# Optimization experiments

Measured on AMD Instinct MI355X. Metric: run time of the kernel, lower is better.

## Reference

```python
import jax, jax.numpy as jnp
import numpy as np

HIDDEN = 4096
N_HEADS = 32
N_KV_HEADS = 8
HEAD_DIM = HIDDEN // N_HEADS  # 128
Q_SIZE = N_HEADS * HEAD_DIM
KV_SIZE = N_KV_HEADS * HEAD_DIM
ROPE_THETA = 10000.0
EPS = 1e-5
SCALE = HEAD_DIM ** -0.5


def _headwise_layernorm(x, weight, eps):
    # x: [B,S,H,D], weight: [H,D]; LayerNorm over last dim (head_dim), fp32 math
    xf = x.astype(jnp.float32)
    mean = xf.mean(-1, keepdims=True)
    var = jnp.square(xf - mean).mean(-1, keepdims=True)
    y = (xf - mean) * jax.lax.rsqrt(var + eps)
    return (weight.astype(jnp.float32) * y).astype(x.dtype)


def _rope_gptj(x, positions):
    # non-neox (GPT-J) style: rotate interleaved pairs. x: [B,S,H,D]
    half = HEAD_DIM // 2
    inv_freq = 1.0 / (ROPE_THETA ** (jnp.arange(0, HEAD_DIM, 2, dtype=jnp.float32) / HEAD_DIM))
    ang = positions.astype(jnp.float32)[..., None] * inv_freq  # [B,S,half]
    cos = jnp.cos(ang)[:, :, None, :]  # [B,S,1,half]
    sin = jnp.sin(ang)[:, :, None, :]
    x1 = x[..., 0::2]
    x2 = x[..., 1::2]
    o1 = x1 * cos - x2 * sin
    o2 = x2 * cos + x1 * sin
    # re-interleave
    out = jnp.stack([o1, o2], axis=-1).reshape(x.shape)
    return out.astype(x.dtype)


def setup_inputs() -> dict:
    key = jax.random.key(0)
    k1, k2, k3, k4 = jax.random.split(key, 4)
    B, S = 2, 2048
    positions = jnp.tile(jnp.arange(S, dtype=jnp.int32)[None, :], (B, 1))
    hidden_states = jax.random.normal(k1, (B, S, HIDDEN), dtype=jnp.float32)
    Wqkv = jax.random.normal(k2, (HIDDEN, Q_SIZE + 2 * KV_SIZE), dtype=jnp.float32) * (HIDDEN ** -0.5)
    Wo = jax.random.normal(k3, (Q_SIZE, HIDDEN), dtype=jnp.float32) * (Q_SIZE ** -0.5)
    kq, kk = jax.random.split(k4)
    q_norm_w = jnp.ones((N_HEADS, HEAD_DIM), jnp.float32) + 0.02 * jax.random.normal(kq, (N_HEADS, HEAD_DIM))
    k_norm_w = jnp.ones((N_KV_HEADS, HEAD_DIM), jnp.float32) + 0.02 * jax.random.normal(kk, (N_KV_HEADS, HEAD_DIM))
    return {"positions": positions, "hidden_states": hidden_states, "Wqkv": Wqkv,
            "q_norm_w": q_norm_w, "k_norm_w": k_norm_w, "Wo": Wo}


def reference(positions, hidden_states, Wqkv, q_norm_w, k_norm_w, Wo):
    B, S, _ = hidden_states.shape
    qkv = hidden_states @ Wqkv  # [B,S,Q+2KV]
    q, k, v = jnp.split(qkv, [Q_SIZE, Q_SIZE + KV_SIZE], axis=-1)
    q = q.reshape(B, S, N_HEADS, HEAD_DIM)
    k = k.reshape(B, S, N_KV_HEADS, HEAD_DIM)
    v = v.reshape(B, S, N_KV_HEADS, HEAD_DIM)
    # per-head qk-norm
    q = _headwise_layernorm(q, q_norm_w, EPS)
    k = _headwise_layernorm(k, k_norm_w, EPS)
    # non-neox RoPE
    q = _rope_gptj(q, positions)
    k = _rope_gptj(k, positions)
    # GQA: repeat kv heads
    n_rep = N_HEADS // N_KV_HEADS
    k = jnp.repeat(k, n_rep, axis=2)  # [B,S,H,D]
    v = jnp.repeat(v, n_rep, axis=2)
    scores = jnp.einsum('bqhd,bkhd->bhqk', q, k) * SCALE
    causal = jnp.tril(jnp.ones((S, S), dtype=bool))
    scores = jnp.where(causal[None, None], scores, jnp.finfo(scores.dtype).min)
    probs = jax.nn.softmax(scores, axis=-1)
    attn = jnp.einsum('bhqk,bkhd->bqhd', probs, v).reshape(B, S, Q_SIZE)
    return attn @ Wo
```

## Files before the change

kernel.cpp:

```cpp
#include <hip/hip_runtime.h>
#include <hip/hip_bf16.h>
#include <cstdint>

typedef unsigned short u16;
typedef unsigned int u32;
typedef __attribute__((ext_vector_type(8))) short bf16x8;
typedef __attribute__((ext_vector_type(4))) float f32x4;
typedef __attribute__((ext_vector_type(16))) float f32x16;
typedef __attribute__((ext_vector_type(4))) unsigned int u32x4;

#define HIDDEN 4096
#define NH 32
#define NKV 8
#define HD 128
#define QSZ 4096
#define KVSZ 1024
#define QKV_N 6144
#define SEQ 2048
#define NB 2
#define NTOK (NB*SEQ)
#define ATT_SCALE 0.08838834764831845f
#define LOG2E 1.4426950408889634f
#define LN_EPS 1e-5f
#define THRD 12.0f

__device__ __forceinline__ u16 f2bf(float f) {
  union { float f; u32 u; } a; a.f = f;
  u32 r = a.u + 0x7fffu + ((a.u >> 16) & 1u);
  return (u16)(r >> 16);
}
__device__ __forceinline__ float bf2f(u16 h) {
  union { u32 u; float f; } a; a.u = ((u32)h) << 16;
  return a.f;
}

__device__ __forceinline__ void gload_lds16(const void* g, void* l) {
  __builtin_amdgcn_global_load_lds(
      (const __attribute__((address_space(1))) void*)g,
      (__attribute__((address_space(3))) void*)l,
      16, 0, 0);
}

__global__ __launch_bounds__(256)
void conv_f32_bf16(const float* __restrict__ in, u16* __restrict__ out, int n8) {
  int i = blockIdx.x * 256 + threadIdx.x;
  if (i >= n8) return;
  const float4* p = (const float4*)in + (size_t)i * 2;
  float4 v0 = p[0], v1 = p[1];
  u32x4 o;
  o.x = (u32)f2bf(v0.x) | ((u32)f2bf(v0.y) << 16);
  o.y = (u32)f2bf(v0.z) | ((u32)f2bf(v0.w) << 16);
  o.z = (u32)f2bf(v1.x) | ((u32)f2bf(v1.y) << 16);
  o.w = (u32)f2bf(v1.z) | ((u32)f2bf(v1.w) << 16);
  ((u32x4*)out)[i] = o;
}

__global__ __launch_bounds__(256)
void transp_f32_bf16(const float* __restrict__ in, u16* __restrict__ out, int R, int C) {
  __shared__ float tile[32][33];
  int c0 = blockIdx.x << 5, r0 = blockIdx.y << 5;
  int tx = threadIdx.x & 31, ty = threadIdx.x >> 5;
  #pragma unroll
  for (int j = 0; j < 32; j += 8)
    tile[ty + j][tx] = in[(long)(r0 + ty + j) * C + c0 + tx];
  __syncthreads();
  #pragma unroll
  for (int j = 0; j < 32; j += 8)
    out[(long)(c0 + ty + j) * R + r0 + tx] = f2bf(tile[tx][ty + j]);
}

template<typename OutT>
__global__ __launch_bounds__(512, 2)
void gemm_bt6(const u16* __restrict__ A, const u16* __restrict__ Bt,
              OutT* __restrict__ C, int N, int K) {
  extern __shared__ char smem[];
  const int t = threadIdx.x;
  const int lane = t & 63, w = t >> 6;
  const int wr = w >> 2, wc = w & 3;
  const int l31 = lane & 31, l7 = lane & 7, g2 = lane >> 5;
  const int bm = blockIdx.y, bn = blockIdx.x;

  const int ciA0 = t, ciA1 = t + 512;
  const u16* AgS0 = A + (long)(bm * 128 + (ciA0 >> 3)) * K + (((ciA0 & 7) ^ ((ciA0 >> 3) & 7)) << 3);
  const u16* AgS1 = A + (long)(bm * 128 + (ciA1 >> 3)) * K + (((ciA1 & 7) ^ ((ciA1 >> 3) & 7)) << 3);
  const u16* BgS0;
  const u16* BgS1;
  const u16* BgS2;
  const u16* BgS3;
  {
    int ci0 = t, ci1 = t + 512, ci2 = t + 1024, ci3 = t + 1536;
    BgS0 = Bt + (long)(bn * 256 + (ci0 >> 3)) * K + (((ci0 & 7) ^ ((ci0 >> 3) & 7)) << 3);
    BgS1 = Bt + (long)(bn * 256 + (ci1 >> 3)) * K + (((ci1 & 7) ^ ((ci1 >> 3) & 7)) << 3);
    BgS2 = Bt + (long)(bn * 256 + (ci2 >> 3)) * K + (((ci2 & 7) ^ ((ci2 >> 3) & 7)) << 3);
    BgS3 = Bt + (long)(bn * 256 + (ci3 >> 3)) * K + (((ci3 & 7) ^ ((ci3 >> 3) & 7)) << 3);
  }
  const int dA0 = (w * 64) * 16;
  const int dA1 = (512 + w * 64) * 16;
  const int dB0 = 16384 + (w * 64) * 16;
  const int dB1 = 16384 + (512 + w * 64) * 16;
  const int dB2 = 16384 + (1024 + w * 64) * 16;
  const int dB3 = 16384 + (1536 + w * 64) * 16;

  const int arow0 = (wr * 64 + l31) * 128;
  const int brow0 = 16384 + (wc * 64 + l31) * 128;

  f32x16 acc[2][2];
  #pragma unroll
  for (int i = 0; i < 2; ++i)
    #pragma unroll
    for (int j = 0; j < 2; ++j)
      #pragma unroll
      for (int r = 0; r < 16; ++r) acc[i][j][r] = 0.f;

  const int nt = K >> 6;
  char* cbase = smem;
  char* nbase = smem + 49152;
  char* sbase = smem + 98304;

  #define STAGE6(dst, koff) { \
    gload_lds16(AgS0 + (koff), dst + dA0);  gload_lds16(AgS1 + (koff), dst + dA1); \
    gload_lds16(BgS0 + (koff), dst + dB0);  gload_lds16(BgS1 + (koff), dst + dB1); \
    gload_lds16(BgS2 + (koff), dst + dB2);  gload_lds16(BgS3 + (koff), dst + dB3); }

  STAGE6(cbase, 0);
  STAGE6(nbase, 64);
  asm volatile("s_waitcnt vmcnt(6)" ::: "memory");
  __builtin_amdgcn_s_barrier();
  __builtin_amdgcn_sched_barrier(0);

  #define READ_KK(dst, kkv) { \
    const int pcb = (((kkv) * 2 + g2) ^ l7) * 16; \
    dst[0] = *(const bf16x8*)(cbase + arow0 + pcb); \
    dst[1] = *(const bf16x8*)(cbase + arow0 + 32 * 128 + pcb); \
    dst[2] = *(const bf16x8*)(cbase + brow0 + pcb); \
    dst[3] = *(const bf16x8*)(cbase + brow0 + 32 * 128 + pcb); }
  #define MFMA_KK(f) { \
    __builtin_amdgcn_s_setprio(1); \
    acc[0][0] = __builtin_amdgcn_mfma_f32_32x32x16_bf16(f[0], f[2], acc[0][0], 0, 0, 0); \
    acc[0][1] = __builtin_amdgcn_mfma_f32_32x32x16_bf16(f[0], f[3], acc[0][1], 0, 0, 0); \
    acc[1][0] = __builtin_amdgcn_mfma_f32_32x32x16_bf16(f[1], f[2], acc[1][0], 0, 0, 0); \
    acc[1][1] = __builtin_amdgcn_mfma_f32_32x32x16_bf16(f[1], f[3], acc[1][1], 0, 0, 0); \
    __builtin_amdgcn_s_setprio(0); }

  for (int tt = 0; tt < nt; ++tt) {
    const long sk = (long)((tt + 2 < nt) ? (tt + 2) : (nt - 1)) * 64;
    STAGE6(sbase, sk);
    bf16x8 fA[4], fB[4], fC[4], fD[4];
    READ_KK(fA, 0);
    READ_KK(fB, 1);
    MFMA_KK(fA);
    READ_KK(fC, 2);
    MFMA_KK(fB);
    READ_KK(fD, 3);
    MFMA_KK(fC);
    MFMA_KK(fD);
    asm volatile("s_waitcnt vmcnt(6)" ::: "memory");
    __builtin_amdgcn_s_barrier();
    __builtin_amdgcn_sched_barrier(0);
    char* tmp = cbase; cbase = nbase; nbase = sbase; sbase = tmp;
  }
  #undef READ_KK
  #undef MFMA_KK
  #undef STAGE6

  #pragma unroll
  for (int mf = 0; mf < 2; ++mf)
    #pragma unroll
    for (int nf = 0; nf < 2; ++nf)
      #pragma unroll
      for (int r = 0; r < 16; ++r) {
        long row = bm * 128 + wr * 64 + mf * 32 + (r & 3) + 8 * (r >> 2) + 4 * g2;
        long col = bn * 256 + wc * 64 + nf * 32 + l31;
        float v = acc[mf][nf][r];
        if constexpr (sizeof(OutT) == 2) C[row * N + col] = f2bf(v);
        else                             C[row * N + col] = v;
      }
}

__device__ __forceinline__ void ln_rope_head(const u16* __restrict__ src,
                                             const float* __restrict__ wgt,
                                             u16* __restrict__ dst,
                                             int lane, float sa, float ca, float scale) {
  u32 xr = *(const u32*)(src + 2 * lane);
  float x1 = bf2f((u16)(xr & 0xffffu)), x2 = bf2f((u16)(xr >> 16));
  float ssum = x1 + x2;
  #pragma unroll
  for (int off = 1; off < 64; off <<= 1) ssum += __shfl_xor(ssum, off);
  float mean = ssum * (1.0f / 128.0f);
  float e1 = x1 - mean, e2 = x2 - mean;
  float vv = e1 * e1 + e2 * e2;
  #pragma unroll
  for (int off = 1; off < 64; off <<= 1) vv += __shfl_xor(vv, off);
  float rstd = rsqrtf(vv * (1.0f / 128.0f) + LN_EPS);
  float y1 = e1 * rstd * wgt[2 * lane];
  float y2 = e2 * rstd * wgt[2 * lane + 1];
  float o1 = (y1 * ca - y2 * sa) * scale;
  float o2 = (y2 * ca + y1 * sa) * scale;
  *(u32*)(dst + 2 * lane) = (u32)f2bf(o1) | ((u32)f2bf(o2) << 16);
}

__global__ __launch_bounds__(512)
void ln_rope(const u16* __restrict__ qkv, const int* __restrict__ pos,
             const float* __restrict__ qw, const float* __restrict__ kw,
             u16* __restrict__ qo, u16* __restrict__ ko) {
  const int s = blockIdx.x, b = blockIdx.y;
  const int t = threadIdx.x, lane = t & 63, w = t >> 6;
  const long base = (long)(b * SEQ + s) * QKV_N;
  const int p = pos[b * SEQ + s];
  const float expo = (float)(2 * lane) * (1.0f / 128.0f);
  const float inv_freq = exp2f(-expo * 13.287712379549449f);
  float sa, ca;
  sincosf((float)p * inv_freq, &sa, &ca);
  #pragma unroll
  for (int hh = 0; hh < 4; ++hh) {
    int h = w + hh * 8;
    ln_rope_head(qkv + base + h * HD, qw + h * HD,
                 qo + (((long)b * NH + h) * SEQ + s) * HD, lane, sa, ca,
                 ATT_SCALE * LOG2E);
  }
  ln_rope_head(qkv + base + QSZ + w * HD, kw + w * HD,
               ko + (((long)b * NKV + w) * SEQ + s) * HD, lane, sa, ca, 1.0f);
}

__global__ __launch_bounds__(256)
void v_transp(const u16* __restrict__ qkv, u16* __restrict__ vt) {
  __shared__ u16 tile[32][33];
  int s0 = blockIdx.x * 32, d0 = blockIdx.y * 32;
  int bk = blockIdx.z;
  int b = bk >> 3, kvh = bk & 7;
  int tx = threadIdx.x & 31, ty = threadIdx.x >> 5;
  const u16* src = qkv + ((long)(b * SEQ) + s0) * QKV_N + QSZ + KVSZ + kvh * HD + d0;
  #pragma unroll
  for (int j = 0; j < 32; j += 8)
    tile[ty + j][tx] = src[(long)(ty + j) * QKV_N + tx];
  __syncthreads();
  u16* dst = vt + (((long)bk) * HD + d0) * SEQ + s0;
  #pragma unroll
  for (int j = 0; j < 32; j += 8)
    dst[(long)(ty + j) * SEQ + tx] = tile[tx][ty + j];
}

__global__ __launch_bounds__(512, 2)
void flash_attn2(const u16* __restrict__ Qg, const u16* __restrict__ Kg,
                 const u16* __restrict__ Vtg, u16* __restrict__ Og) {
  const int lin = blockIdx.x;
  const int b = lin >> 8;
  const int rem = lin & 255;
  const int h = rem >> 3;
  const int q3 = rem & 7;
  const int qt = b ? (7 - q3) : q3;
  const int kvh = h >> 2;
  const int t = threadIdx.x, lane = t & 63, w = t >> 6;
  const int hh = lane >> 5, l31 = lane & 31;
  const int wq0 = qt * 256 + w * 32;
  const int q = wq0 + l31;

  __shared__ u16 Klds[2][64 * 128];
  __shared__ u16 Vlds[2][128 * 64];

  const u16* Qbase = Qg + (((long)b * NH + h) * SEQ + q) * HD + hh * 8;
  bf16x8 qf[8];
  #pragma unroll
  for (int ks = 0; ks < 8; ++ks) qf[ks] = *(const bf16x8*)(Qbase + ks * 16);

  f32x16 o[4];
  #pragma unroll
  for (int i = 0; i < 4; ++i)
    #pragma unroll
    for (int r = 0; r < 16; ++r) o[i][r] = 0.f;
  float m = -1e30f, l = 0.f;

  const u16* Kbase = Kg + ((long)b * NKV + kvh) * (long)SEQ * HD;
  const u16* Vtbase = Vtg + ((long)b * NKV + kvh) * (long)HD * SEQ;
  const int nt = qt * 4 + 4;

  auto STAGE = [&](int buf, int kt) {
    const int kv0 = kt * 64;
    #pragma unroll
    for (int i = 0; i < 2; ++i) {
      int c = t + i * 512;
      int kv = c >> 4, cc = c & 15;
      int cl = (cc & 8) | ((cc ^ kv) & 7);
      gload_lds16(Kbase + (long)(kv0 + kv) * HD + cl * 8,
                  (char*)(&Klds[buf][0]) + (i * 512 + w * 64) * 16);
    }
    #pragma unroll
    for (int i = 0; i < 2; ++i) {
      int c = t + i * 512;
      int d = c >> 3, cc = c & 7;
      int cl = cc ^ (d & 7);
      gload_lds16(Vtbase + (long)d * SEQ + kv0 + cl * 8,
                  (char*)(&Vlds[buf][0]) + (i * 512 + w * 64) * 16);
    }
  };

  STAGE(0, 0);
  __syncthreads();
  int cur = 0;
  for (int kt = 0; kt < nt; ++kt) {
    const int kv0 = kt * 64;
    if (kt + 1 < nt) STAGE(cur ^ 1, kt + 1);
    if (kv0 <= wq0 + 31) {
      const char* Kb = (const char*)(&Klds[cur][0]);
      const char* Vb = (const char*)(&Vlds[cur][0]);
      f32x16 st[2];
      #pragma unroll
      for (int tt = 0; tt < 2; ++tt)
        #pragma unroll
        for (int r = 0; r < 16; ++r) st[tt][r] = 0.f;
      __builtin_amdgcn_s_setprio(1);
      #pragma unroll
      for (int tt = 0; tt < 2; ++tt) {
        if (kv0 + tt * 32 <= wq0 + 31) {
          #pragma unroll
          for (int ks = 0; ks < 8; ++ks) {
            int ch = ks * 2 + hh;
            int pc = (ch & 8) | ((ch ^ l31) & 7);
            bf16x8 kf = *(const bf16x8*)(Kb + (tt * 32 + l31) * 256 + pc * 16);
            st[tt] = __builtin_amdgcn_mfma_f32_32x32x16_bf16(kf, qf[ks], st[tt], 0, 0, 0);
          }
        }
      }
      __builtin_amdgcn_s_setprio(0);
      if (kv0 + 63 > wq0) {
        #pragma unroll
        for (int tt = 0; tt < 2; ++tt)
          #pragma unroll
          for (int r = 0; r < 16; ++r) {
            int kva = kv0 + tt * 32 + (r & 3) + 8 * (r >> 2) + 4 * hh;
            if (kva > q) st[tt][r] = -1e30f;
          }
      }
      float p0 = -1e30f, p1 = -1e30f, p2 = -1e30f, p3 = -1e30f;
      #pragma unroll
      for (int tt = 0; tt < 2; ++tt)
        #pragma unroll
        for (int r = 0; r < 16; r += 4) {
          p0 = fmaxf(p0, st[tt][r]);
          p1 = fmaxf(p1, st[tt][r + 1]);
          p2 = fmaxf(p2, st[tt][r + 2]);
          p3 = fmaxf(p3, st[tt][r + 3]);
        }
      float mx = fmaxf(fmaxf(p0, p1), fmaxf(p2, p3));
      mx = fmaxf(mx, __shfl_xor(mx, 32));
      if (!__all(mx - m <= THRD)) {
        float mn = fmaxf(m, mx);
        float sc = exp2f(m - mn);
        m = mn;
        float scr[16];
        #pragma unroll
        for (int r = 0; r < 16; ++r)
          scr[r] = __shfl(sc, (r & 3) + 8 * (r >> 2) + 4 * hh);
        #pragma unroll
        for (int db = 0; db < 4; ++db)
          #pragma unroll
          for (int r = 0; r < 16; ++r) o[db][r] *= scr[r];
        l *= sc;
      }
      float s0 = 0.f, s1 = 0.f, s2 = 0.f, s3 = 0.f;
      #pragma unroll
      for (int tt = 0; tt < 2; ++tt)
        #pragma unroll
        for (int r = 0; r < 16; r += 4) {
          float e0 = exp2f(st[tt][r] - m);
          float e1 = exp2f(st[tt][r + 1] - m);
          float e2 = exp2f(st[tt][r + 2] - m);
          float e3 = exp2f(st[tt][r + 3] - m);
          st[tt][r] = e0; st[tt][r + 1] = e1; st[tt][r + 2] = e2; st[tt][r + 3] = e3;
          s0 += e0; s1 += e1; s2 += e2; s3 += e3;
        }
      float rs = (s0 + s1) + (s2 + s3);
      rs += __shfl_xor(rs, 32);
      l += rs;
      bf16x8 pa[4];
      #pragma unroll
      for (int k4 = 0; k4 < 4; ++k4) {
        int s8 = (k4 & 1) * 8, tt = k4 >> 1;
        u32 x0 = (u32)f2bf(st[tt][s8 + 0]) | ((u32)f2bf(st[tt][s8 + 1]) << 16);
        u32 x1 = (u32)f2bf(st[tt][s8 + 2]) | ((u32)f2bf(st[tt][s8 + 3]) << 16);
        u32 y0 = (u32)f2bf(st[tt][s8 + 4]) | ((u32)f2bf(st[tt][s8 + 5]) << 16);
        u32 y1 = (u32)f2bf(st[tt][s8 + 6]) | ((u32)f2bf(st[tt][s8 + 7]) << 16);
        u32 x0s = (u32)__shfl_xor((int)x0, 32), x1s = (u32)__shfl_xor((int)x1, 32);
        u32 y0s = (u32)__shfl_xor((int)y0, 32), y1s = (u32)__shfl_xor((int)y1, 32);
        union { u32 u[4]; bf16x8 v; } pk;
        pk.u[0] = hh ? y0s : x0;
        pk.u[1] = hh ? y1s : x1;
        pk.u[2] = hh ? y0 : x0s;
        pk.u[3] = hh ? y1 : x1s;
        pa[k4] = pk.v;
      }
      __builtin_amdgcn_s_setprio(1);
      #pragma unroll
      for (int k4 = 0; k4 < 4; ++k4)
        #pragma unroll
        for (int db = 0; db < 4; ++db) {
          int ch = k4 * 2 + hh;
          int pcc = ch ^ (l31 & 7);
          bf16x8 vf = *(const bf16x8*)(Vb + (db * 32 + l31) * 128 + pcc * 16);
          o[db] = __builtin_amdgcn_mfma_f32_32x32x16_bf16(pa[k4], vf, o[db], 0, 0, 0);
        }
      __builtin_amdgcn_s_setprio(0);
    }
    __syncthreads();
    cur ^= 1;
  }
  float linv = 1.0f / l;
  float li[16];
  #pragma unroll
  for (int r = 0; r < 16; ++r)
    li[r] = __shfl(linv, (r & 3) + 8 * (r >> 2) + 4 * hh);
  #pragma unroll
  for (int db = 0; db < 4; ++db)
    #pragma unroll
    for (int r = 0; r < 16; ++r) {
      int qr = wq0 + (r & 3) + 8 * (r >> 2) + 4 * hh;
      Og[((long)b * SEQ + qr) * QSZ + h * HD + db * 32 + l31] = f2bf(o[db][r] * li[r]);
    }
}

extern "C" void kernel_launch(void* const* d_in, const int* in_sizes, int n_in,
                              void* d_out, int out_size, void* d_ws, size_t ws_size,
                              hipStream_t stream) {
  const int*   positions = (const int*)d_in[0];
  const float* hidden    = (const float*)d_in[1];
  const float* Wqkv      = (const float*)d_in[2];
  const float* qnw       = (const float*)d_in[3];
  const float* knw       = (const float*)d_in[4];
  const float* Wo        = (const float*)d_in[5];
  float* out = (float*)d_out;
  char* ws = (char*)d_ws;
  const size_t MB = 1024 * 1024;
  u16* hbf   = (u16*)(ws + 0);
  u16* WqkvT = (u16*)(ws + 32 * MB);
  u16* qkvb  = (u16*)(ws + 80 * MB);
  u16* q_arr = (u16*)(ws + 0);
  u16* k_arr = (u16*)(ws + 32 * MB);
  u16* vt_arr= (u16*)(ws + 40 * MB);
  u16* WoT   = (u16*)(ws + 48 * MB);
  u16* Oarr  = (u16*)(ws + 80 * MB);

  const int GEMM_LDS = 3 * 49152;
  (void)hipFuncSetAttribute((const void*)&gemm_bt6<u16>,
        hipFuncAttributeMaxDynamicSharedMemorySize, GEMM_LDS);
  (void)hipFuncSetAttribute((const void*)&gemm_bt6<float>,
        hipFuncAttributeMaxDynamicSharedMemorySize, GEMM_LDS);

  conv_f32_bf16<<<dim3(NTOK * HIDDEN / 8 / 256), 256, 0, stream>>>(hidden, hbf, NTOK * HIDDEN / 8);
  transp_f32_bf16<<<dim3(QKV_N / 32, HIDDEN / 32), 256, 0, stream>>>(Wqkv, WqkvT, HIDDEN, QKV_N);
  gemm_bt6<u16><<<dim3(QKV_N / 256, NTOK / 128), 512, GEMM_LDS, stream>>>(hbf, WqkvT, qkvb, QKV_N, HIDDEN);
  ln_rope<<<dim3(SEQ, NB), 512, 0, stream>>>(qkvb, positions, qnw, knw, q_arr, k_arr);
  v_transp<<<dim3(SEQ / 32, HD / 32, NB * NKV), 256, 0, stream>>>(qkvb, vt_arr);
  transp_f32_bf16<<<dim3(HIDDEN / 32, QSZ / 32), 256, 0, stream>>>(Wo, WoT, QSZ, HIDDEN);
  flash_attn2<<<dim3(512), 512, 0, stream>>>(q_arr, k_arr, vt_arr, Oarr);
  gemm_bt6<float><<<dim3(HIDDEN / 256, NTOK / 128), 512, GEMM_LDS, stream>>>(Oarr, WoT, out, HIDDEN, QSZ);
}
```

Baseline: 584.7 us.

## Split GEMM main loop into two ping-pong phases with interleaved loads and barriers

Restructures the GEMM inner loop into two half-steps. Each half issues half of the global-to-LDS prefetch loads together with LDS fragment reads, then runs a barrier-delimited MFMA cluster at raised priority, in the style of a ping-pong schedule across the waves of two co-resident blocks. The aim is to spread memory issue across the iteration and overlap it with matrix math. The cost is two extra workgroup barriers per iteration and more sensitivity to scheduling.

```diff
diff --git a/kernel.cpp b/kernel.cpp
--- a/kernel.cpp
+++ b/kernel.cpp
@@ -71,7 +71,7 @@
 
 template<typename OutT>
 __global__ __launch_bounds__(512, 2)
-void gemm_bt6(const u16* __restrict__ A, const u16* __restrict__ Bt,
+void gemm_bt7(const u16* __restrict__ A, const u16* __restrict__ Bt,
               OutT* __restrict__ C, int N, int K) {
   extern __shared__ char smem[];
   const int t = threadIdx.x;
@@ -135,28 +135,43 @@
     dst[2] = *(const bf16x8*)(cbase + brow0 + pcb); \
     dst[3] = *(const bf16x8*)(cbase + brow0 + 32 * 128 + pcb); }
   #define MFMA_KK(f) { \
-    __builtin_amdgcn_s_setprio(1); \
     acc[0][0] = __builtin_amdgcn_mfma_f32_32x32x16_bf16(f[0], f[2], acc[0][0], 0, 0, 0); \
     acc[0][1] = __builtin_amdgcn_mfma_f32_32x32x16_bf16(f[0], f[3], acc[0][1], 0, 0, 0); \
     acc[1][0] = __builtin_amdgcn_mfma_f32_32x32x16_bf16(f[1], f[2], acc[1][0], 0, 0, 0); \
-    acc[1][1] = __builtin_amdgcn_mfma_f32_32x32x16_bf16(f[1], f[3], acc[1][1], 0, 0, 0); \
-    __builtin_amdgcn_s_setprio(0); }
+    acc[1][1] = __builtin_amdgcn_mfma_f32_32x32x16_bf16(f[1], f[3], acc[1][1], 0, 0, 0); }
 
   for (int tt = 0; tt < nt; ++tt) {
     const long sk = (long)((tt + 2 < nt) ? (tt + 2) : (nt - 1)) * 64;
-    STAGE6(sbase, sk);
-    bf16x8 fA[4], fB[4], fC[4], fD[4];
+    bf16x8 fA[4], fB[4];
     READ_KK(fA, 0);
     READ_KK(fB, 1);
+    gload_lds16(AgS0 + sk, sbase + dA0);
+    gload_lds16(AgS1 + sk, sbase + dA1);
+    gload_lds16(BgS0 + sk, sbase + dB0);
+    __builtin_amdgcn_sched_barrier(0);
+    __builtin_amdgcn_s_barrier();
+    __builtin_amdgcn_sched_barrier(0);
+    __builtin_amdgcn_s_setprio(1);
     MFMA_KK(fA);
-    READ_KK(fC, 2);
     MFMA_KK(fB);
-    READ_KK(fD, 3);
-    MFMA_KK(fC);
-    MFMA_KK(fD);
+    __builtin_amdgcn_s_setprio(0);
+    __builtin_amdgcn_sched_barrier(0);
+    __builtin_amdgcn_s_barrier();
+    READ_KK(fA, 2);
+    READ_KK(fB, 3);
+    gload_lds16(BgS1 + sk, sbase + dB1);
+    gload_lds16(BgS2 + sk, sbase + dB2);
+    gload_lds16(BgS3 + sk, sbase + dB3);
     asm volatile("s_waitcnt vmcnt(6)" ::: "memory");
+    __builtin_amdgcn_sched_barrier(0);
     __builtin_amdgcn_s_barrier();
     __builtin_amdgcn_sched_barrier(0);
+    __builtin_amdgcn_s_setprio(1);
+    MFMA_KK(fA);
+    MFMA_KK(fB);
+    __builtin_amdgcn_s_setprio(0);
+    __builtin_amdgcn_sched_barrier(0);
+    __builtin_amdgcn_s_barrier();
     char* tmp = cbase; cbase = nbase; nbase = sbase; sbase = tmp;
   }
   #undef READ_KK
@@ -440,17 +455,17 @@
   u16* Oarr  = (u16*)(ws + 80 * MB);
 
   const int GEMM_LDS = 3 * 49152;
-  (void)hipFuncSetAttribute((const void*)&gemm_bt6<u16>,
+  (void)hipFuncSetAttribute((const void*)&gemm_bt7<u16>,
         hipFuncAttributeMaxDynamicSharedMemorySize, GEMM_LDS);
-  (void)hipFuncSetAttribute((const void*)&gemm_bt6<float>,
+  (void)hipFuncSetAttribute((const void*)&gemm_bt7<float>,
         hipFuncAttributeMaxDynamicSharedMemorySize, GEMM_LDS);
 
   conv_f32_bf16<<<dim3(NTOK * HIDDEN / 8 / 256), 256, 0, stream>>>(hidden, hbf, NTOK * HIDDEN / 8);
   transp_f32_bf16<<<dim3(QKV_N / 32, HIDDEN / 32), 256, 0, stream>>>(Wqkv, WqkvT, HIDDEN, QKV_N);
-  gemm_bt6<u16><<<dim3(QKV_N / 256, NTOK / 128), 512, GEMM_LDS, stream>>>(hbf, WqkvT, qkvb, QKV_N, HIDDEN);
+  gemm_bt7<u16><<<dim3(QKV_N / 256, NTOK / 128), 512, GEMM_LDS, stream>>>(hbf, WqkvT, qkvb, QKV_N, HIDDEN);
   ln_rope<<<dim3(SEQ, NB), 512, 0, stream>>>(qkvb, positions, qnw, knw, q_arr, k_arr);
   v_transp<<<dim3(SEQ / 32, HD / 32, NB * NKV), 256, 0, stream>>>(qkvb, vt_arr);
   transp_f32_bf16<<<dim3(HIDDEN / 32, QSZ / 32), 256, 0, stream>>>(Wo, WoT, QSZ, HIDDEN);
   flash_attn2<<<dim3(512), 512, 0, stream>>>(q_arr, k_arr, vt_arr, Oarr);
-  gemm_bt6<float><<<dim3(HIDDEN / 256, NTOK / 128), 512, GEMM_LDS, stream>>>(Oarr, WoT, out, HIDDEN, QSZ);
-}
+  gemm_bt7<float><<<dim3(HIDDEN / 256, NTOK / 128), 512, GEMM_LDS, stream>>>(Oarr, WoT, out, HIDDEN, QSZ);
+}
```

Result: no change. 594.1 us (+1.6%).

## Add 256x256 double-buffered output GEMM and pair causal q-tiles in attention

Applied to the files above, without the earlier changes.

Adds a new gemm_bt4 kernel for the output projection. It uses 256x256 tiles with double buffering, and each wave computes a 128x64 block, which raises data reuse per LDS load. The attention kernel now processes two causal q-tiles per block: a long one (7-qp) and a short one (qp). This balances the work and halves the grid to 256 blocks. The risks are more register pressure in the bigger GEMM, lower occupancy (the grid becomes 16x16=256 blocks), and less latency hiding in attention from the smaller grid.

```diff
diff --git a/kernel.cpp b/kernel.cpp
--- a/kernel.cpp
+++ b/kernel.cpp
@@ -128,13 +128,13 @@
   __builtin_amdgcn_s_barrier();
   __builtin_amdgcn_sched_barrier(0);
 
-  #define READ_KK(dst, kkv) { \
+  #define READ_KK6(dst, kkv) { \
     const int pcb = (((kkv) * 2 + g2) ^ l7) * 16; \
     dst[0] = *(const bf16x8*)(cbase + arow0 + pcb); \
     dst[1] = *(const bf16x8*)(cbase + arow0 + 32 * 128 + pcb); \
     dst[2] = *(const bf16x8*)(cbase + brow0 + pcb); \
     dst[3] = *(const bf16x8*)(cbase + brow0 + 32 * 128 + pcb); }
-  #define MFMA_KK(f) { \
+  #define MFMA_KK6(f) { \
     __builtin_amdgcn_s_setprio(1); \
     acc[0][0] = __builtin_amdgcn_mfma_f32_32x32x16_bf16(f[0], f[2], acc[0][0], 0, 0, 0); \
     acc[0][1] = __builtin_amdgcn_mfma_f32_32x32x16_bf16(f[0], f[3], acc[0][1], 0, 0, 0); \
@@ -146,21 +146,21 @@
     const long sk = (long)((tt + 2 < nt) ? (tt + 2) : (nt - 1)) * 64;
     STAGE6(sbase, sk);
     bf16x8 fA[4], fB[4], fC[4], fD[4];
-    READ_KK(fA, 0);
-    READ_KK(fB, 1);
-    MFMA_KK(fA);
-    READ_KK(fC, 2);
-    MFMA_KK(fB);
-    READ_KK(fD, 3);
-    MFMA_KK(fC);
-    MFMA_KK(fD);
+    READ_KK6(fA, 0);
+    READ_KK6(fB, 1);
+    MFMA_KK6(fA);
+    READ_KK6(fC, 2);
+    MFMA_KK6(fB);
+    READ_KK6(fD, 3);
+    MFMA_KK6(fC);
+    MFMA_KK6(fD);
     asm volatile("s_waitcnt vmcnt(6)" ::: "memory");
     __builtin_amdgcn_s_barrier();
     __builtin_amdgcn_sched_barrier(0);
     char* tmp = cbase; cbase = nbase; nbase = sbase; sbase = tmp;
   }
-  #undef READ_KK
-  #undef MFMA_KK
+  #undef READ_KK6
+  #undef MFMA_KK6
   #undef STAGE6
 
   #pragma unroll
@@ -170,6 +170,113 @@
       #pragma unroll
       for (int r = 0; r < 16; ++r) {
         long row = bm * 128 + wr * 64 + mf * 32 + (r & 3) + 8 * (r >> 2) + 4 * g2;
+        long col = bn * 256 + wc * 64 + nf * 32 + l31;
+        float v = acc[mf][nf][r];
+        if constexpr (sizeof(OutT) == 2) C[row * N + col] = f2bf(v);
+        else                             C[row * N + col] = v;
+      }
+}
+
+template<typename OutT>
+__global__ __launch_bounds__(512, 2)
+void gemm_bt4(const u16* __restrict__ A, const u16* __restrict__ Bt,
+              OutT* __restrict__ C, int N, int K) {
+  extern __shared__ char smem[];
+  const int t = threadIdx.x;
+  const int lane = t & 63, w = t >> 6;
+  const int wr = w >> 2, wc = w & 3;
+  const int l31 = lane & 31, g2 = lane >> 5;
+  const int bm = blockIdx.y, bn = blockIdx.x;
+
+  const u16* pA[4]; const u16* pB[4];
+  int dS[4];
+  #pragma unroll
+  for (int i = 0; i < 4; ++i) {
+    int ci = t + i * 512;
+    int row = ci >> 3;
+    int c = (ci & 7) ^ (row & 7);
+    pA[i] = A  + (long)(bm * 256 + row) * K + (c << 3);
+    pB[i] = Bt + (long)(bn * 256 + row) * K + (c << 3);
+    dS[i] = (i * 512 + w * 64) * 16;
+  }
+
+  const int arowB = (wr * 128 + l31) * 128;
+  const int browB = 32768 + (wc * 64 + l31) * 128;
+
+  f32x16 acc[4][2];
+  #pragma unroll
+  for (int i = 0; i < 4; ++i)
+    #pragma unroll
+    for (int j = 0; j < 2; ++j)
+      #pragma unroll
+      for (int r = 0; r < 16; ++r) acc[i][j][r] = 0.f;
+
+  const int nt = K >> 6;
+  char* cb = smem;
+  char* sb = smem + 65536;
+
+  #pragma unroll
+  for (int i = 0; i < 4; ++i) gload_lds16(pA[i], cb + dS[i]);
+  #pragma unroll
+  for (int i = 0; i < 4; ++i) gload_lds16(pB[i], cb + 32768 + dS[i]);
+  asm volatile("s_waitcnt vmcnt(0)" ::: "memory");
+  __builtin_amdgcn_s_barrier();
+  __builtin_amdgcn_sched_barrier(0);
+
+  #define READ_KK4(dst, kkv) { \
+    const int pcb = ((((kkv) * 2 + g2)) ^ (l31 & 7)) << 4; \
+    dst[0] = *(const bf16x8*)(cb + arowB + pcb); \
+    dst[1] = *(const bf16x8*)(cb + arowB + 4096 + pcb); \
+    dst[2] = *(const bf16x8*)(cb + arowB + 8192 + pcb); \
+    dst[3] = *(const bf16x8*)(cb + arowB + 12288 + pcb); \
+    dst[4] = *(const bf16x8*)(cb + browB + pcb); \
+    dst[5] = *(const bf16x8*)(cb + browB + 4096 + pcb); }
+  #define MFMA_KK4(f) { \
+    __builtin_amdgcn_s_setprio(1); \
+    acc[0][0] = __builtin_amdgcn_mfma_f32_32x32x16_bf16(f[0], f[4], acc[0][0], 0, 0, 0); \
+    acc[0][1] = __builtin_amdgcn_mfma_f32_32x32x16_bf16(f[0], f[5], acc[0][1], 0, 0, 0); \
+    acc[1][0] = __builtin_amdgcn_mfma_f32_32x32x16_bf16(f[1], f[4], acc[1][0], 0, 0, 0); \
+    acc[1][1] = __builtin_amdgcn_mfma_f32_32x32x16_bf16(f[1], f[5], acc[1][1], 0, 0, 0); \
+    acc[2][0] = __builtin_amdgcn_mfma_f32_32x32x16_bf16(f[2], f[4], acc[2][0], 0, 0, 0); \
+    acc[2][1] = __builtin_amdgcn_mfma_f32_32x32x16_bf16(f[2], f[5], acc[2][1], 0, 0, 0); \
+    acc[3][0] = __builtin_amdgcn_mfma_f32_32x32x16_bf16(f[3], f[4], acc[3][0], 0, 0, 0); \
+    acc[3][1] = __builtin_amdgcn_mfma_f32_32x32x16_bf16(f[3], f[5], acc[3][1], 0, 0, 0); \
+    __builtin_amdgcn_s_setprio(0); }
+
+  for (int tt = 0; tt < nt; ++tt) {
+    const long sk = (long)((tt + 1 < nt) ? (tt + 1) : (nt - 1)) * 64;
+    bf16x8 f0[6], f1[6];
+    READ_KK4(f0, 0);
+    gload_lds16(pA[0] + sk, sb + dS[0]);
+    gload_lds16(pA[1] + sk, sb + dS[1]);
+    READ_KK4(f1, 1);
+    gload_lds16(pA[2] + sk, sb + dS[2]);
+    gload_lds16(pA[3] + sk, sb + dS[3]);
+    MFMA_KK4(f0);
+    gload_lds16(pB[0] + sk, sb + 32768 + dS[0]);
+    gload_lds16(pB[1] + sk, sb + 32768 + dS[1]);
+    MFMA_KK4(f1);
+    READ_KK4(f0, 2);
+    gload_lds16(pB[2] + sk, sb + 32768 + dS[2]);
+    gload_lds16(pB[3] + sk, sb + 32768 + dS[3]);
+    MFMA_KK4(f0);
+    READ_KK4(f1, 3);
+    MFMA_KK4(f1);
+    asm volatile("s_waitcnt vmcnt(0)" ::: "memory");
+    __builtin_amdgcn_s_barrier();
+    __builtin_amdgcn_sched_barrier(0);
+    char* tmp = cb; cb = sb; sb = tmp;
+  }
+  #undef READ_KK4
+  #undef MFMA_KK4
+
+  #pragma unroll
+  for (int mf = 0; mf < 4; ++mf)
+    #pragma unroll
+    for (int nf = 0; nf < 2; ++nf)
+      #pragma unroll
+      for (int r = 0; r < 16; ++r) {
+        long row = bm * 256 + wr * 128 + mf * 32 + (r & 3) + 8 * (r >> 2) + 4 * g2;
         long col = bn * 256 + wc * 64 + nf * 32 + l31;
         float v = acc[mf][nf][r];
         if constexpr (sizeof(OutT) == 2) C[row * N + col] = f2bf(v);
@@ -241,38 +348,22 @@
 }
 
 __global__ __launch_bounds__(512, 2)
-void flash_attn2(const u16* __restrict__ Qg, const u16* __restrict__ Kg,
+void flash_attn3(const u16* __restrict__ Qg, const u16* __restrict__ Kg,
                  const u16* __restrict__ Vtg, u16* __restrict__ Og) {
   const int lin = blockIdx.x;
-  const int b = lin >> 8;
-  const int rem = lin & 255;
-  const int h = rem >> 3;
-  const int q3 = rem & 7;
-  const int qt = b ? (7 - q3) : q3;
+  const int b = lin >> 7;
+  const int rem = lin & 127;
+  const int h = rem >> 2;
+  const int qp = rem & 3;
   const int kvh = h >> 2;
   const int t = threadIdx.x, lane = t & 63, w = t >> 6;
   const int hh = lane >> 5, l31 = lane & 31;
-  const int wq0 = qt * 256 + w * 32;
-  const int q = wq0 + l31;
 
   __shared__ u16 Klds[2][64 * 128];
   __shared__ u16 Vlds[2][128 * 64];
 
-  const u16* Qbase = Qg + (((long)b * NH + h) * SEQ + q) * HD + hh * 8;
-  bf16x8 qf[8];
-  #pragma unroll
-  for (int ks = 0; ks < 8; ++ks) qf[ks] = *(const bf16x8*)(Qbase + ks * 16);
-
-  f32x16 o[4];
-  #pragma unroll
-  for (int i = 0; i < 4; ++i)
-    #pragma unroll
-    for (int r = 0; r < 16; ++r) o[i][r] = 0.f;
-  float m = -1e30f, l = 0.f;
-
   const u16* Kbase = Kg + ((long)b * NKV + kvh) * (long)SEQ * HD;
   const u16* Vtbase = Vtg + ((long)b * NKV + kvh) * (long)HD * SEQ;
-  const int nt = qt * 4 + 4;
 
   auto STAGE = [&](int buf, int kt) {
     const int kv0 = kt * 64;
@@ -294,128 +385,147 @@
     }
   };
 
-  STAGE(0, 0);
-  __syncthreads();
-  int cur = 0;
-  for (int kt = 0; kt < nt; ++kt) {
-    const int kv0 = kt * 64;
-    if (kt + 1 < nt) STAGE(cur ^ 1, kt + 1);
-    if (kv0 <= wq0 + 31) {
-      const char* Kb = (const char*)(&Klds[cur][0]);
-      const char* Vb = (const char*)(&Vlds[cur][0]);
-      f32x16 st[2];
+  for (int seg = 0; seg < 2; ++seg) {
+    const int qt = seg ? qp : (7 - qp);
+    const int wq0 = qt * 256 + w * 32;
+    const int q = wq0 + l31;
+    const u16* Qbase = Qg + (((long)b * NH + h) * SEQ + q) * HD + hh * 8;
+    bf16x8 qf[8];
+    #pragma unroll
+    for (int ks = 0; ks < 8; ++ks) qf[ks] = *(const bf16x8*)(Qbase + ks * 16);
+
+    f32x16 o[4];
+    #pragma unroll
+    for (int i = 0; i < 4; ++i)
       #pragma unroll
-      for (int tt = 0; tt < 2; ++tt)
+      for (int r = 0; r < 16; ++r) o[i][r] = 0.f;
+    float m = -1e30f, l = 0.f;
+    const int nt = qt * 4 + 4;
+
+    __syncthreads();
+    STAGE(0, 0);
+    __syncthreads();
+    int cur = 0;
+    for (int kt = 0; kt < nt; ++kt) {
+      const int kv0 = kt * 64;
+      if (kt + 1 < nt) STAGE(cur ^ 1, kt + 1);
+      if (kv0 <= wq0 + 31) {
+        const char* Kb = (const char*)(&Klds[cur][0]);
+        const char* Vb = (const char*)(&Vlds[cur][0]);
+        f32x16 st[2];
         #pragma unroll
-        for (int r = 0; r < 16; ++r) st[tt][r] = 0.f;
-      __builtin_amdgcn_s_setprio(1);
-      #pragma unroll
-      for (int tt = 0; tt < 2; ++tt) {
-        if (kv0 + tt * 32 <= wq0 + 31) {
-          #pragma unroll
-          for (int ks = 0; ks < 8; ++ks) {
-            int ch = ks * 2 + hh;
-            int pc = (ch & 8) | ((ch ^ l31) & 7);
-            bf16x8 kf = *(const bf16x8*)(Kb + (tt * 32 + l31) * 256 + pc * 16);
-            st[tt] = __builtin_amdgcn_mfma_f32_32x32x16_bf16(kf, qf[ks], st[tt], 0, 0, 0);
+        for (int tt = 0; tt < 2; ++tt)
+          #pragma unroll
+          for (int r = 0; r < 16; ++r) st[tt][r] = 0.f;
+        __builtin_amdgcn_s_setprio(1);
+        #pragma unroll
+        for (int tt = 0; tt < 2; ++tt) {
+          if (kv0 + tt * 32 <= wq0 + 31) {
+            #pragma unroll
+            for (int ks = 0; ks < 8; ++ks) {
+              int ch = ks * 2 + hh;
+              int pc = (ch & 8) | ((ch ^ l31) & 7);
+              bf16x8 kf = *(const bf16x8*)(Kb + (tt * 32 + l31) * 256 + pc * 16);
+              st[tt] = __builtin_amdgcn_mfma_f32_32x32x16_bf16(kf, qf[ks], st[tt], 0, 0, 0);
+            }
           }
         }
-      }
-      __builtin_amdgcn_s_setprio(0);
-      if (kv0 + 63 > wq0) {
+        __builtin_amdgcn_s_setprio(0);
+        if (kv0 + 63 > wq0) {
+          #pragma unroll
+          for (int tt = 0; tt < 2; ++tt)
+            #pragma unroll
+            for (int r = 0; r < 16; ++r) {
+              int kva = kv0 + tt * 32 + (r & 3) + 8 * (r >> 2) + 4 * hh;
+              if (kva > q) st[tt][r] = -1e30f;
+            }
+        }
+        float p0 = -1e30f, p1 = -1e30f, p2 = -1e30f, p3 = -1e30f;
         #pragma unroll
         for (int tt = 0; tt < 2; ++tt)
           #pragma unroll
-          for (int r = 0; r < 16; ++r) {
-            int kva = kv0 + tt * 32 + (r & 3) + 8 * (r >> 2) + 4 * hh;
-            if (kva > q) st[tt][r] = -1e30f;
+          for (int r = 0; r < 16; r += 4) {
+            p0 = fmaxf(p0, st[tt][r]);
+            p1 = fmaxf(p1, st[tt][r + 1]);
+            p2 = fmaxf(p2, st[tt][r + 2]);
+            p3 = fmaxf(p3, st[tt][r + 3]);
           }
+        float mx = fmaxf(fmaxf(p0, p1), fmaxf(p2, p3));
+        mx = fmaxf(mx, __shfl_xor(mx, 32));
+        if (!__all(mx - m <= THRD)) {
+          float mn = fmaxf(m, mx);
+          float sc = exp2f(m - mn);
+          m = mn;
+          float scr[16];
+          #pragma unroll
+          for (int r = 0; r < 16; ++r)
+            scr[r] = __shfl(sc, (r & 3) + 8 * (r >> 2) + 4 * hh);
+          #pragma unroll
+          for (int db = 0; db < 4; ++db)
+            #pragma unroll
+            for (int r = 0; r < 16; ++r) o[db][r] *= scr[r];
+          l *= sc;
+        }
+        float s0 = 0.f, s1 = 0.f, s2 = 0.f, s3 = 0.f;
+        #pragma unroll
+        for (int tt = 0; tt < 2; ++tt)
+          #pragma unroll
+          for (int r = 0; r < 16; r += 4) {
+            float e0 = exp2f(st[tt][r] - m);
+            float e1 = exp2f(st[tt][r + 1] - m);
+            float e2 = exp2f(st[tt][r + 2] - m);
+            float e3 = exp2f(st[tt][r + 3] - m);
+            st[tt][r] = e0; st[tt][r + 1] = e1; st[tt][r + 2] = e2; st[tt][r + 3] = e3;
+            s0 += e0; s1 += e1; s2 += e2; s3 += e3;
+          }
+        float rs = (s0 + s1) + (s2 + s3);
+        rs += __shfl_xor(rs, 32);
+        l += rs;
+        bf16x8 pa[4];
+        #pragma unroll
+        for (int k4 = 0; k4 < 4; ++k4) {
+          int s8 = (k4 & 1) * 8, tt = k4 >> 1;
+          u32 x0 = (u32)f2bf(st[tt][s8 + 0]) | ((u32)f2bf(st[tt][s8 + 1]) << 16);
+          u32 x1 = (u32)f2bf(st[tt][s8 + 2]) | ((u32)f2bf(st[tt][s8 + 3]) << 16);
+          u32 y0 = (u32)f2bf(st[tt][s8 + 4]) | ((u32)f2bf(st[tt][s8 + 5]) << 16);
+          u32 y1 = (u32)f2bf(st[tt][s8 + 6]) | ((u32)f2bf(st[tt][s8 + 7]) << 16);
+          u32 x0s = (u32)__shfl_xor((int)x0, 32), x1s = (u32)__shfl_xor((int)x1, 32);
+          u32 y0s = (u32)__shfl_xor((int)y0, 32), y1s = (u32)__shfl_xor((int)y1, 32);
+          union { u32 u[4]; bf16x8 v; } pk;
+          pk.u[0] = hh ? y0s : x0;
+          pk.u[1] = hh ? y1s : x1;
+          pk.u[2] = hh ? y0 : x0s;
+          pk.u[3] = hh ? y1 : x1s;
+          pa[k4] = pk.v;
+        }
+        __builtin_amdgcn_s_setprio(1);
+        #pragma unroll
+        for (int k4 = 0; k4 < 4; ++k4)
+          #pragma unroll
+          for (int db = 0; db < 4; ++db) {
+            int ch = k4 * 2 + hh;
+            int pcc = ch ^ (l31 & 7);
+            bf16x8 vf = *(const bf16x8*)(Vb + (db * 32 + l31) * 128 + pcc * 16);
+            o[db] = __builtin_amdgcn_mfma_f32_32x32x16_bf16(pa[k4], vf, o[db], 0, 0, 0);
+          }
+        __builtin_amdgcn_s_setprio(0);
       }
-      float p0 = -1e30f, p1 = -1e30f, p2 = -1e30f, p3 = -1e30f;
+      __syncthreads();
+      cur ^= 1;
+    }
+    float linv = 1.0f / l;
+    float li[16];
+    #pragma unroll
+    for (int r = 0; r < 16; ++r)
+      li[r] = __shfl(linv, (r & 3) + 8 * (r >> 2) + 4 * hh);
+    #pragma unroll
+    for (int db = 0; db < 4; ++db)
       #pragma unroll
-      for (int tt = 0; tt < 2; ++tt)
-        #pragma unroll
-        for (int r = 0; r < 16; r += 4) {
-          p0 = fmaxf(p0, st[tt][r]);
-          p1 = fmaxf(p1, st[tt][r + 1]);
-          p2 = fmaxf(p2, st[tt][r + 2]);
-          p3 = fmaxf(p3, st[tt][r + 3]);
-        }
-      float mx = fmaxf(fmaxf(p0, p1), fmaxf(p2, p3));
-      mx = fmaxf(mx, __shfl_xor(mx, 32));
-      if (!__all(mx - m <= THRD)) {
-        float mn = fmaxf(m, mx);
-        float sc = exp2f(m - mn);
-        m = mn;
-        float scr[16];
-        #pragma unroll
-        for (int r = 0; r < 16; ++r)
-          scr[r] = __shfl(sc, (r & 3) + 8 * (r >> 2) + 4 * hh);
-        #pragma unroll
-        for (int db = 0; db < 4; ++db)
-          #pragma unroll
-          for (int r = 0; r < 16; ++r) o[db][r] *= scr[r];
-        l *= sc;
+      for (int r = 0; r < 16; ++r) {
+        int qr = wq0 + (r & 3) + 8 * (r >> 2) + 4 * hh;
+        Og[((long)b * SEQ + qr) * QSZ + h * HD + db * 32 + l31] = f2bf(o[db][r] * li[r]);
       }
-      float s0 = 0.f, s1 = 0.f, s2 = 0.f, s3 = 0.f;
-      #pragma unroll
-      for (int tt = 0; tt < 2; ++tt)
-        #pragma unroll
-        for (int r = 0; r < 16; r += 4) {
-          float e0 = exp2f(st[tt][r] - m);
-          float e1 = exp2f(st[tt][r + 1] - m);
-          float e2 = exp2f(st[tt][r + 2] - m);
-          float e3 = exp2f(st[tt][r + 3] - m);
-          st[tt][r] = e0; st[tt][r + 1] = e1; st[tt][r + 2] = e2; st[tt][r + 3] = e3;
-          s0 += e0; s1 += e1; s2 += e2; s3 += e3;
-        }
-      float rs = (s0 + s1) + (s2 + s3);
-      rs += __shfl_xor(rs, 32);
-      l += rs;
-      bf16x8 pa[4];
-      #pragma unroll
-      for (int k4 = 0; k4 < 4; ++k4) {
-        int s8 = (k4 & 1) * 8, tt = k4 >> 1;
-        u32 x0 = (u32)f2bf(st[tt][s8 + 0]) | ((u32)f2bf(st[tt][s8 + 1]) << 16);
-        u32 x1 = (u32)f2bf(st[tt][s8 + 2]) | ((u32)f2bf(st[tt][s8 + 3]) << 16);
-        u32 y0 = (u32)f2bf(st[tt][s8 + 4]) | ((u32)f2bf(st[tt][s8 + 5]) << 16);
-        u32 y1 = (u32)f2bf(st[tt][s8 + 6]) | ((u32)f2bf(st[tt][s8 + 7]) << 16);
-        u32 x0s = (u32)__shfl_xor((int)x0, 32), x1s = (u32)__shfl_xor((int)x1, 32);
-        u32 y0s = (u32)__shfl_xor((int)y0, 32), y1s = (u32)__shfl_xor((int)y1, 32);
-        union { u32 u[4]; bf16x8 v; } pk;
-        pk.u[0] = hh ? y0s : x0;
-        pk.u[1] = hh ? y1s : x1;
-        pk.u[2] = hh ? y0 : x0s;
-        pk.u[3] = hh ? y1 : x1s;
-        pa[k4] = pk.v;
-      }
-      __builtin_amdgcn_s_setprio(1);
-      #pragma unroll
-      for (int k4 = 0; k4 < 4; ++k4)
-        #pragma unroll
-        for (int db = 0; db < 4; ++db) {
-          int ch = k4 * 2 + hh;
-          int pcc = ch ^ (l31 & 7);
-          bf16x8 vf = *(const bf16x8*)(Vb + (db * 32 + l31) * 128 + pcc * 16);
-          o[db] = __builtin_amdgcn_mfma_f32_32x32x16_bf16(pa[k4], vf, o[db], 0, 0, 0);
-        }
-      __builtin_amdgcn_s_setprio(0);
-    }
-    __syncthreads();
-    cur ^= 1;
   }
-  float linv = 1.0f / l;
-  float li[16];
-  #pragma unroll
-  for (int r = 0; r < 16; ++r)
-    li[r] = __shfl(linv, (r & 3) + 8 * (r >> 2) + 4 * hh);
-  #pragma unroll
-  for (int db = 0; db < 4; ++db)
-    #pragma unroll
-    for (int r = 0; r < 16; ++r) {
-      int qr = wq0 + (r & 3) + 8 * (r >> 2) + 4 * hh;
-      Og[((long)b * SEQ + qr) * QSZ + h * HD + db * 32 + l31] = f2bf(o[db][r] * li[r]);
-    }
 }
 
 extern "C" void kernel_launch(void* const* d_in, const int* in_sizes, int n_in,
@@ -439,18 +549,19 @@
   u16* WoT   = (u16*)(ws + 48 * MB);
   u16* Oarr  = (u16*)(ws + 80 * MB);
 
-  const int GEMM_LDS = 3 * 49152;
+  const int GEMM6_LDS = 3 * 49152;
+  const int GEMM4_LDS = 2 * 65536;
   (void)hipFuncSetAttribute((const void*)&gemm_bt6<u16>,
-        hipFuncAttributeMaxDynamicSharedMemorySize, GEMM_LDS);
-  (void)hipFuncSetAttribute((const void*)&gemm_bt6<float>,
-        hipFuncAttributeMaxDynamicSharedMemorySize, GEMM_LDS);
+        hipFuncAttributeMaxDynamicSharedMemorySize, GEMM6_LDS);
+  (void)hipFuncSetAttribute((const void*)&gemm_bt4<float>,
+        hipFuncAttributeMaxDynamicSharedMemorySize, GEMM4_LDS);
 
   conv_f32_bf16<<<dim3(NTOK * HIDDEN / 8 / 256), 256, 0, stream>>>(hidden, hbf, NTOK * HIDDEN / 8);
   transp_f32_bf16<<<dim3(QKV_N / 32, HIDDEN / 32), 256, 0, stream>>>(Wqkv, WqkvT, HIDDEN, QKV_N);
-  gemm_bt6<u16><<<dim3(QKV_N / 256, NTOK / 128), 512, GEMM_LDS, stream>>>(hbf, WqkvT, qkvb, QKV_N, HIDDEN);
+  gemm_bt6<u16><<<dim3(QKV_N / 256, NTOK / 128), 512, GEMM6_LDS, stream>>>(hbf, WqkvT, qkvb, QKV_N, HIDDEN);
   ln_rope<<<dim3(SEQ, NB), 512, 0, stream>>>(qkvb, positions, qnw, knw, q_arr, k_arr);
   v_transp<<<dim3(SEQ / 32, HD / 32, NB * NKV), 256, 0, stream>>>(qkvb, vt_arr);
   transp_f32_bf16<<<dim3(HIDDEN / 32, QSZ / 32), 256, 0, stream>>>(Wo, WoT, QSZ, HIDDEN);
-  flash_attn2<<<dim3(512), 512, 0, stream>>>(q_arr, k_arr, vt_arr, Oarr);
-  gemm_bt6<float><<<dim3(HIDDEN / 256, NTOK / 128), 512, GEMM_LDS, stream>>>(Oarr, WoT, out, HIDDEN, QSZ);
-}
+  flash_attn3<<<dim3(256), 512, 0, stream>>>(q_arr, k_arr, vt_arr, Oarr);
+  gemm_bt4<float><<<dim3(HIDDEN / 256, NTOK / 256), 512, GEMM4_LDS, stream>>>(Oarr, WoT, out, HIDDEN, QSZ);
+}
```

After: 565.3 us (median of 2 runs). 1.03x faster.
